# Kernel optimization log

Measured on AMD Instinct MI355X. Metric: run time of the kernel, lower is better.

Reference implementation:

```python
import jax, jax.numpy as jnp
import numpy as np

D_MODEL, N_LEVELS, N_HEADS, N_POINTS = 256, 4, 8, 4
SHAPES = [(100, 100), (50, 50), (25, 25), (13, 13)]  # (H, W) per level


def setup_inputs() -> dict:
    key = jax.random.key(0)
    ks = jax.random.split(key, 8)
    N = 2
    C = D_MODEL
    Len_in = sum(h * w for h, w in SHAPES)
    Lq = Len_in  # encoder self-attention
    query = jax.random.normal(ks[0], (N, Lq, C), jnp.float32)
    reference_points = jax.random.uniform(ks[1], (N, Lq, N_LEVELS, 2), dtype=jnp.float32)
    input_flatten = jax.random.normal(ks[2], (N, Len_in, C), jnp.float32)
    input_spatial_shapes = np.array(SHAPES, dtype=np.int64)
    areas = input_spatial_shapes[:, 0] * input_spatial_shapes[:, 1]
    input_level_start_index = np.concatenate([[0], np.cumsum(areas)[:-1]]).astype(np.int64)
    s = 1.0 / np.sqrt(C)
    Wv = jax.random.uniform(ks[3], (C, C), jnp.float32, -s, s)
    bv = jnp.zeros((C,), jnp.float32)
    # sampling_offsets: small random weight + the module's grid bias init
    Woff = jax.random.normal(ks[4], (N_HEADS * N_LEVELS * N_POINTS * 2, C), jnp.float32) * 0.01
    thetas = jnp.arange(N_HEADS, dtype=jnp.float32) * (2.0 * np.pi / N_HEADS)
    grid = jnp.stack([jnp.cos(thetas), jnp.sin(thetas)], -1)  # (M,2)
    grid = grid / jnp.max(jnp.abs(grid), axis=-1, keepdims=True)
    grid = jnp.tile(grid[:, None, None, :], (1, N_LEVELS, N_POINTS, 1))
    grid = grid * (jnp.arange(N_POINTS, dtype=jnp.float32) + 1.0)[None, None, :, None]
    boff = grid.reshape(-1)
    Wa = jax.random.normal(ks[5], (N_HEADS * N_LEVELS * N_POINTS, C), jnp.float32) * 0.02
    ba = jnp.zeros((N_HEADS * N_LEVELS * N_POINTS,), jnp.float32)
    Wo = jax.random.uniform(ks[6], (C, C), jnp.float32, -s, s)
    bo = jnp.zeros((C,), jnp.float32)
    return {
        'query': query, 'reference_points': reference_points, 'input_flatten': input_flatten,
        'input_spatial_shapes': input_spatial_shapes, 'input_level_start_index': input_level_start_index,
        'Wv': Wv, 'bv': bv, 'Woff': Woff, 'boff': boff, 'Wa': Wa, 'ba': ba, 'Wo': Wo, 'bo': bo,
    }


def _msda_forward(query, reference_points, input_flatten, shapes, starts,
                  Wv, bv, Woff, boff, Wa, ba, Wo, bo):
    N, Lq, C = query.shape
    M, L, P = N_HEADS, N_LEVELS, N_POINTS
    D = C // M
    value = (input_flatten @ Wv.T + bv).reshape(N, -1, M, D)  # (N, Len_in, M, D)
    off = (query @ Woff.T + boff).reshape(N, Lq, M, L, P, 2)
    attn = jax.nn.softmax((query @ Wa.T + ba).reshape(N, Lq, M, L * P), axis=-1)
    attn = attn.reshape(N, Lq, M, L, P)
    # offset_normalizer = (W_l, H_l)
    norm = jnp.asarray(shapes[:, ::-1].copy(), jnp.float32)  # (L, 2)
    loc = reference_points[:, :, None, :, None, :] + off / norm[None, None, None, :, None, :]
    grids = 2.0 * loc - 1.0  # (N, Lq, M, L, P, 2), grid_sample convention
    out = jnp.zeros((N, Lq, M, D), query.dtype)
    for l in range(L):
        H, W = int(shapes[l, 0]), int(shapes[l, 1])
        s0 = int(starts[l])
        v = value[:, s0:s0 + H * W]  # (N, H*W, M, D)
        # align_corners=False unnormalization
        gx = ((grids[:, :, :, l, :, 0] + 1.0) * W - 1.0) / 2.0  # (N, Lq, M, P)
        gy = ((grids[:, :, :, l, :, 1] + 1.0) * H - 1.0) / 2.0
        x0 = jnp.floor(gx); y0 = jnp.floor(gy)
        fx = gx - x0;       fy = gy - y0
        x0i = x0.astype(jnp.int32); y0i = y0.astype(jnp.int32)

        def gather(iy, ix):
            valid = (iy >= 0) & (iy < H) & (ix >= 0) & (ix < W)
            lin = jnp.clip(iy, 0, H - 1) * W + jnp.clip(ix, 0, W - 1)  # (N, Lq, M, P)
            lin2 = lin.transpose(0, 1, 3, 2).reshape(N, Lq * P, M)
            g = jnp.take_along_axis(v, lin2[..., None], axis=1)  # (N, Lq*P, M, D)
            g = g.reshape(N, Lq, P, M, D).transpose(0, 1, 3, 2, 4)  # (N, Lq, M, P, D)
            return g * valid[..., None]  # zero padding outside

        s00 = gather(y0i, x0i)
        s01 = gather(y0i, x0i + 1)
        s10 = gather(y0i + 1, x0i)
        s11 = gather(y0i + 1, x0i + 1)
        sampled = (s00 * ((1 - fy) * (1 - fx))[..., None] + s01 * ((1 - fy) * fx)[..., None]
                   + s10 * (fy * (1 - fx))[..., None] + s11 * (fy * fx)[..., None])
        out = out + jnp.einsum('nqmp,nqmpd->nqmd', attn[:, :, :, l], sampled)
    out = out.reshape(N, Lq, C)
    return out @ Wo.T + bo


def reference(query, reference_points, input_flatten, input_spatial_shapes, input_level_start_index,
              Wv, bv, Woff, boff, Wa, ba, Wo, bo):
    shapes = np.asarray(input_spatial_shapes)
    starts = np.asarray(input_level_start_index)
    return _msda_forward(query, reference_points, input_flatten, shapes, starts,
                         Wv, bv, Woff, boff, Wa, ba, Wo, bo)
```

## Files before the change

### kernel.cpp

```cpp
#include <hip/hip_runtime.h>
#include <math.h>

#define NB   2
#define LQ   13294
#define NROWS (NB*LQ)
#define CDIM 256
#define HSLICES (NROWS + 1)
#define HS32 ((size_t)HSLICES * 32)

typedef unsigned short u16;
typedef unsigned int   u32;
typedef short bf16x8 __attribute__((ext_vector_type(8)));
typedef float f32x4  __attribute__((ext_vector_type(4)));
typedef float f32x2  __attribute__((ext_vector_type(2)));

struct alignas(8) U16x4 { u16 x, y, z, w; };

__device__ __forceinline__ u16 f2bf(float f) {
    u32 u = __builtin_bit_cast(u32, f);
    u += 0x7FFFu + ((u >> 16) & 1u);
    return (u16)(u >> 16);
}

__device__ __forceinline__ u32 cvtpk(float a, float b) {
    u32 d;
    asm("v_cvt_pk_bf16_f32 %0, %1, %2" : "=v"(d) : "v"(a), "v"(b));
    return d;
}

__device__ __forceinline__ void gload_lds16(const void* g, void* l) {
    __builtin_amdgcn_global_load_lds(
        (__attribute__((address_space(1))) void*)g,
        (__attribute__((address_space(3))) void*)l, 16, 0, 0);
}

__device__ __forceinline__ f32x2 bfpair(u32 u) {
    union { u32 w[2]; f32x2 v; } x;
    x.w[0] = u << 16;
    x.w[1] = u & 0xFFFF0000u;
    return x.v;
}

__device__ __forceinline__ void core_f32src(
    const float* __restrict__ A, const float* __restrict__ Bf, int M, int row0,
    u16* As, u16* Bs, f32x4 (&acc)[4][4]) {
    const int tid  = threadIdx.x;
    const int lane = tid & 63;
    const int wave = tid >> 6;
    const int ln16 = lane & 15;
    const int kq   = lane >> 4;
    const int wr   = (wave >> 1) * 64;
    const int wc   = (wave & 1) * 64;

    #pragma unroll
    for (int kt = 0; kt < 4; ++kt) {
        const int k0 = kt * 64;
        #pragma unroll
        for (int it = 0; it < 4; ++it) {
            int chunk = it * 256 + tid;
            int row = chunk >> 3;
            int ch  = chunk & 7;
            int dst = row * 64 + ((ch ^ (row & 7)) * 8);
            int gra = min(row0 + row, M - 1);
            const float* pa = A + (size_t)gra * 256 + k0 + ch * 8;
            float4 a0 = *(const float4*)pa;
            float4 a1 = *(const float4*)(pa + 4);
            uint4 ua;
            ua.x = cvtpk(a0.x, a0.y); ua.y = cvtpk(a0.z, a0.w);
            ua.z = cvtpk(a1.x, a1.y); ua.w = cvtpk(a1.z, a1.w);
            *(uint4*)&As[dst] = ua;
            const float* pb = Bf + (size_t)row * 256 + k0 + ch * 8;
            float4 b0 = *(const float4*)pb;
            float4 b1 = *(const float4*)(pb + 4);
            uint4 ub;
            ub.x = cvtpk(b0.x, b0.y); ub.y = cvtpk(b0.z, b0.w);
            ub.z = cvtpk(b1.x, b1.y); ub.w = cvtpk(b1.z, b1.w);
            *(uint4*)&Bs[dst] = ub;
        }
        __syncthreads();
        #pragma unroll
        for (int kf = 0; kf < 2; ++kf) {
            const int ck = kf * 4 + kq;
            bf16x8 a[4], b[4];
            #pragma unroll
            for (int i = 0; i < 4; ++i) {
                int r = wr + i * 16 + ln16;
                a[i] = *(const bf16x8*)&As[r * 64 + ((ck ^ (r & 7)) * 8)];
                int c = wc + i * 16 + ln16;
                b[i] = *(const bf16x8*)&Bs[c * 64 + ((ck ^ (c & 7)) * 8)];
            }
            #pragma unroll
            for (int i = 0; i < 4; ++i)
                #pragma unroll
                for (int j = 0; j < 4; ++j)
                    acc[i][j] = __builtin_amdgcn_mfma_f32_16x16x32_bf16(
                        a[i], b[j], acc[i][j], 0, 0, 0);
        }
        __syncthreads();
    }
}

__device__ __forceinline__ void core_mixed(
    const u16* __restrict__ A, const float* __restrict__ Bf, int M, int row0,
    u16* As, u16* Bs, f32x4 (&acc)[4][4]) {
    const int tid  = threadIdx.x;
    const int lane = tid & 63;
    const int wave = tid >> 6;
    const int ln16 = lane & 15;
    const int kq   = lane >> 4;
    const int wr   = (wave >> 1) * 64;
    const int wc   = (wave & 1) * 64;

    #pragma unroll
    for (int kt = 0; kt < 4; ++kt) {
        const int k0 = kt * 64;
        #pragma unroll
        for (int it = 0; it < 4; ++it) {
            int chunk = it * 256 + tid;
            int row = chunk >> 3;
            int ch  = chunk & 7;
            int chs = (ch ^ (row & 7)) * 8;
            int gra = min(row0 + row, M - 1);
            gload_lds16(A + (size_t)gra * 256 + k0 + chs, As + chunk * 8);
            const float* pb = Bf + (size_t)row * 256 + k0 + ch * 8;
            float4 b0 = *(const float4*)pb;
            float4 b1 = *(const float4*)(pb + 4);
            uint4 ub;
            ub.x = cvtpk(b0.x, b0.y); ub.y = cvtpk(b0.z, b0.w);
            ub.z = cvtpk(b1.x, b1.y); ub.w = cvtpk(b1.z, b1.w);
            *(uint4*)&Bs[row * 64 + chs] = ub;
        }
        __syncthreads();
        #pragma unroll
        for (int kf = 0; kf < 2; ++kf) {
            const int ck = kf * 4 + kq;
            bf16x8 a[4], b[4];
            #pragma unroll
            for (int i = 0; i < 4; ++i) {
                int r = wr + i * 16 + ln16;
                a[i] = *(const bf16x8*)&As[r * 64 + ((ck ^ (r & 7)) * 8)];
                int c = wc + i * 16 + ln16;
                b[i] = *(const bf16x8*)&Bs[c * 64 + ((ck ^ (c & 7)) * 8)];
            }
            #pragma unroll
            for (int i = 0; i < 4; ++i)
                #pragma unroll
                for (int j = 0; j < 4; ++j)
                    acc[i][j] = __builtin_amdgcn_mfma_f32_16x16x32_bf16(
                        a[i], b[j], acc[i][j], 0, 0, 0);
        }
        __syncthreads();
    }
}

__global__ __launch_bounds__(256, 3)
void gemm_front(const float* __restrict__ query, const float* __restrict__ inflat,
                const float* __restrict__ Wv, const float* __restrict__ Woff,
                const float* __restrict__ Wa, const float* __restrict__ bv,
                const float* __restrict__ boff, const float* __restrict__ ba,
                u16* __restrict__ value, float* __restrict__ offb,
                float* __restrict__ logit, int M) {
    __shared__ u16 As[128 * 64];
    __shared__ u16 Bs[128 * 64];
    const int s    = blockIdx.x;
    const int row0 = blockIdx.y * 128;
    const float* A  = (s < 2) ? inflat : query;
    const float* Bf = (s == 0) ? Wv
                    : (s == 1) ? Wv + 32768
                    : (s == 2) ? Woff
                    : (s == 3) ? Woff + 32768
                    : Wa;
    const float* bias = (s < 2) ? bv + s * 128
                      : (s < 4) ? boff + (s - 2) * 128
                      : ba;

    f32x4 acc[4][4] = {};
    core_f32src(A, Bf, M, row0, As, Bs, acc);

    const int lane = threadIdx.x & 63;
    const int wave = threadIdx.x >> 6;
    const int ln16 = lane & 15, kq = lane >> 4;
    const int wr = (wave >> 1) * 64, wc = (wave & 1) * 64;
    #pragma unroll
    for (int j = 0; j < 4; ++j) {
        int lc = wc + j * 16 + ln16;
        float bj = bias[lc];
        #pragma unroll
        for (int i = 0; i < 4; ++i) {
            #pragma unroll
            for (int r = 0; r < 4; ++r) {
                int gr = row0 + wr + i * 16 + kq * 4 + r;
                if (gr < M) {
                    float o = acc[i][j][r] + bj;
                    if (s < 2) {
                        int c = s * 128 + lc;
                        value[(size_t)(c >> 5) * HS32 + (size_t)gr * 32 + (c & 31)] = f2bf(o);
                    } else if (s < 4)
                        offb[(size_t)gr * 256 + (s - 2) * 128 + lc] = o;
                    else
                        logit[(size_t)gr * 128 + lc] = o;
                }
            }
        }
    }
    if (s == 0 && blockIdx.y == 0) {
        int tt = threadIdx.x;
        value[(size_t)(tt >> 5) * HS32 + (size_t)NROWS * 32 + (tt & 31)] = 0;
    }
}

__global__ __launch_bounds__(256, 3)
void gemm_out(const u16* __restrict__ A, const float* __restrict__ Wo,
              const float* __restrict__ bias, float* __restrict__ C, int M) {
    __shared__ u16 As[128 * 64];
    __shared__ u16 Bs[128 * 64];
    const int s    = blockIdx.x;
    const int row0 = blockIdx.y * 128;
    const float* Bf = Wo + (size_t)s * 32768;

    f32x4 acc[4][4] = {};
    core_mixed(A, Bf, M, row0, As, Bs, acc);

    const int lane = threadIdx.x & 63;
    const int wave = threadIdx.x >> 6;
    const int ln16 = lane & 15, kq = lane >> 4;
    const int wr = (wave >> 1) * 64, wc = (wave & 1) * 64;
    #pragma unroll
    for (int j = 0; j < 4; ++j) {
        int gc = s * 128 + wc + j * 16 + ln16;
        float bj = bias[gc];
        #pragma unroll
        for (int i = 0; i < 4; ++i) {
            #pragma unroll
            for (int r = 0; r < 4; ++r) {
                int gr = row0 + wr + i * 16 + kq * 4 + r;
                if (gr < M) C[(size_t)gr * 256 + gc] = acc[i][j][r] + bj;
            }
        }
    }
}

__global__ __launch_bounds__(256)
void msda_sample(const u16* __restrict__ value,
                 const float* __restrict__ refpts,
                 const float* __restrict__ off,
                 const float* __restrict__ logits,
                 u16* __restrict__ tmp) {
    __shared__ float sAw[4][8][16];
    __shared__ int   sLin[4][8][16][2];
    __shared__ float sW[4][8][16][4];

    const int t  = threadIdx.x;
    const int qb = blockIdx.x * 4;

    if (t < 32) {
        const int qi = t >> 3, m = t & 7;
        const float* lg = logits + (size_t)(qb + qi) * 128 + m * 16;
        float e[16];
        float mx = -1e30f;
        #pragma unroll
        for (int i = 0; i < 16; ++i) { e[i] = lg[i]; mx = fmaxf(mx, e[i]); }
        float s = 0.f;
        #pragma unroll
        for (int i = 0; i < 16; ++i) { e[i] = __expf(e[i] - mx); s += e[i]; }
        const float inv = 1.f / s;
        #pragma unroll
        for (int i = 0; i < 16; ++i) sAw[qi][m][i] = e[i] * inv;
    }
    __syncthreads();

    #pragma unroll
    for (int j2 = 0; j2 < 2; ++j2) {
        const int job = t + j2 * 256;
        const int qi = job >> 7;
        const int m  = (job >> 4) & 7;
        const int p  = job & 15;
        const int l  = p >> 2, pp = p & 3;
        const int q  = qb + qi;
        const int n  = (q >= LQ) ? 1 : 0;

        const int W = (l == 0) ? 100 : (l == 1) ? 50 : (l == 2) ? 25 : 13;
        const int H = W;
        const int st = (l == 0) ? 0 : (l == 1) ? 10000 : (l == 2) ? 12500 : 13125;
        const float invW = (l == 0) ? 0.01f : (l == 1) ? 0.02f
                         : (l == 2) ? 0.04f : (1.f / 13.f);

        const float rx = refpts[(size_t)q * 8 + l * 2 + 0];
        const float ry = refpts[(size_t)q * 8 + l * 2 + 1];
        const float ox = off[(size_t)q * 256 + m * 32 + (l * 4 + pp) * 2 + 0];
        const float oy = off[(size_t)q * 256 + m * 32 + (l * 4 + pp) * 2 + 1];

        const float locx = rx + ox * invW;
        const float locy = ry + oy * invW;
        const float grx = 2.f * locx - 1.f;
        const float gry = 2.f * locy - 1.f;
        const float gx = ((grx + 1.f) * (float)W - 1.f) * 0.5f;
        const float gy = ((gry + 1.f) * (float)H - 1.f) * 0.5f;
        const float x0f = floorf(gx), y0f = floorf(gy);
        const float fx = gx - x0f, fy = gy - y0f;
        const int x0 = (int)x0f, y0 = (int)y0f;
        const int x1 = x0 + 1, y1 = y0 + 1;

        const int cx0 = min(max(x0, 0), W - 1);
        const int cx1 = min(max(x1, 0), W - 1);
        const int cy0 = min(max(y0, 0), H - 1);
        const int cy1 = min(max(y1, 0), H - 1);
        const bool vx0 = (x0 >= 0) & (x0 < W);
        const bool vx1 = (x1 >= 0) & (x1 < W);
        const bool vy0 = (y0 >= 0) & (y0 < H);
        const bool vy1 = (y1 >= 0) & (y1 < H);

        const float aw = sAw[qi][m][p];
        const int base = n * LQ + st;
        const float w00 = (vy0 & vx0) ? aw * (1.f - fy) * (1.f - fx) : 0.f;
        const float w01 = (vy0 & vx1) ? aw * (1.f - fy) * fx         : 0.f;
        const float w10 = (vy1 & vx0) ? aw * fy * (1.f - fx)         : 0.f;
        const float w11 = (vy1 & vx1) ? aw * fy * fx                 : 0.f;
        const bool fold = (x0 < 0);
        sLin[qi][m][p][0] = base + cy0 * W + cx0;
        sLin[qi][m][p][1] = base + cy1 * W + cx0;
        sW[qi][m][p][0] = fold ? w01 : w00;
        sW[qi][m][p][1] = fold ? 0.f : w01;
        sW[qi][m][p][2] = fold ? w11 : w10;
        sW[qi][m][p][3] = fold ? 0.f : w11;
    }
    __syncthreads();

    const int qi = t >> 6;
    const int m  = (t >> 3) & 7;
    const int e  = t & 7;
    const int xh = e >> 2;
    const int c4 = e & 3;
    const int q  = qb + qi;
    const char* vb = (const char*)value + (size_t)m * (HS32 * 2);
    const u32 eoff = (u32)e * 16u;

    f32x2 a2[4] = {{0.f, 0.f}, {0.f, 0.f}, {0.f, 0.f}, {0.f, 0.f}};
    #pragma unroll
    for (int p = 0; p < 16; ++p) {
        int2   rb = *(const int2*)  &sLin[qi][m][p][0];
        float4 w4 = *(const float4*)&sW  [qi][m][p][0];
        uint4 r0 = *(const uint4*)(vb + ((u32)rb.x * 64u + eoff));
        uint4 r1 = *(const uint4*)(vb + ((u32)rb.y * 64u + eoff));
        const float wa = xh ? w4.y : w4.x;
        const float wb_ = xh ? w4.w : w4.z;
        f32x2 wa2 = {wa, wa};
        f32x2 wb2 = {wb_, wb_};
        a2[0] += wa2 * bfpair(r0.x); a2[1] += wa2 * bfpair(r0.y);
        a2[2] += wa2 * bfpair(r0.z); a2[3] += wa2 * bfpair(r0.w);
        a2[0] += wb2 * bfpair(r1.x); a2[1] += wb2 * bfpair(r1.y);
        a2[2] += wb2 * bfpair(r1.z); a2[3] += wb2 * bfpair(r1.w);
    }
    #pragma unroll
    for (int k = 0; k < 4; ++k) {
        a2[k].x += __shfl_xor(a2[k].x, 4);
        a2[k].y += __shfl_xor(a2[k].y, 4);
    }
    if (xh == 0) {
        uint4 o;
        o.x = (u32)f2bf(a2[0].x) | ((u32)f2bf(a2[0].y) << 16);
        o.y = (u32)f2bf(a2[1].x) | ((u32)f2bf(a2[1].y) << 16);
        o.z = (u32)f2bf(a2[2].x) | ((u32)f2bf(a2[2].y) << 16);
        o.w = (u32)f2bf(a2[3].x) | ((u32)f2bf(a2[3].y) << 16);
        *(uint4*)((char*)tmp + ((u32)q * 512u + (u32)m * 64u + (u32)c4 * 16u)) = o;
    }
}

extern "C" void kernel_launch(void* const* d_in, const int* in_sizes, int n_in,
                              void* d_out, int out_size, void* d_ws, size_t ws_size,
                              hipStream_t stream) {
    const float* query  = (const float*)d_in[0];
    const float* refpts = (const float*)d_in[1];
    const float* inflat = (const float*)d_in[2];
    const float* Wv   = (const float*)d_in[5];
    const float* bv   = (const float*)d_in[6];
    const float* Woff = (const float*)d_in[7];
    const float* boff = (const float*)d_in[8];
    const float* Wa   = (const float*)d_in[9];
    const float* ba   = (const float*)d_in[10];
    const float* Wo   = (const float*)d_in[11];
    const float* bo   = (const float*)d_in[12];
    float* out = (float*)d_out;

    char* ws = (char*)d_ws;
    constexpr size_t SZ16  = (size_t)NROWS * 256 * 2;
    constexpr size_t SZVAL = ((size_t)HSLICES * 512 + 4095) & ~(size_t)4095;
    constexpr size_t SZ32  = (size_t)NROWS * 256 * 4;
    u16*   tmp   = (u16*)(ws);
    u16*   value = (u16*)(ws + SZ16);
    float* offb  = (float*)(ws + SZ16 + SZVAL);
    float* logit = (float*)(ws + SZ16 + SZVAL + SZ32);

    const int RG = (NROWS + 127) / 128;

    gemm_front<<<dim3(5, RG), dim3(256), 0, stream>>>(
        query, inflat, Wv, Woff, Wa, bv, boff, ba, value, offb, logit, NROWS);

    hipLaunchKernelGGL(msda_sample, dim3(NROWS / 4), dim3(256), 0, stream,
                       value, refpts, offb, logit, tmp);

    gemm_out<<<dim3(2, RG), dim3(256), 0, stream>>>(
        tmp, Wo, bo, out, NROWS);
}
```

Baseline: 223.3 us.

## Pre-convert inputs and weights to bf16, use async LDS loads in GEMMs

```diff
diff --git a/kernel.cpp b/kernel.cpp
--- a/kernel.cpp
+++ b/kernel.cpp
@@ -22,12 +22,6 @@
     return (u16)(u >> 16);
 }
 
-__device__ __forceinline__ u32 cvtpk(float a, float b) {
-    u32 d;
-    asm("v_cvt_pk_bf16_f32 %0, %1, %2" : "=v"(d) : "v"(a), "v"(b));
-    return d;
-}
-
 __device__ __forceinline__ void gload_lds16(const void* g, void* l) {
     __builtin_amdgcn_global_load_lds(
         (__attribute__((address_space(1))) void*)g,
@@ -41,8 +35,37 @@
     return x.v;
 }
 
-__device__ __forceinline__ void core_f32src(
-    const float* __restrict__ A, const float* __restrict__ Bf, int M, int row0,
+__global__ __launch_bounds__(256)
+void prep_all(const float4* __restrict__ query, const float4* __restrict__ inflat,
+              const float* __restrict__ Wv, const float* __restrict__ Woff,
+              const float* __restrict__ Wa, const float* __restrict__ Wo,
+              u16* __restrict__ qb, u16* __restrict__ ib,
+              u16* __restrict__ wb) {
+    const int b = blockIdx.x;
+    const int t = threadIdx.x;
+    if (b < 6647) {
+        int i = b * 256 + t;
+        float4 v = query[i];
+        U16x4 o{f2bf(v.x), f2bf(v.y), f2bf(v.z), f2bf(v.w)};
+        *(U16x4*)&qb[(size_t)i * 4] = o;
+    } else if (b < 13294) {
+        int i = (b - 6647) * 256 + t;
+        float4 v = inflat[i];
+        U16x4 o{f2bf(v.x), f2bf(v.y), f2bf(v.z), f2bf(v.w)};
+        *(U16x4*)&ib[(size_t)i * 4] = o;
+    } else {
+        int i = (b - 13294) * 256 + t;
+        float v;
+        if      (i <  65536) v = Wv[i];
+        else if (i < 131072) v = Woff[i - 65536];
+        else if (i < 163840) v = Wa[i - 131072];
+        else                 v = Wo[i - 163840];
+        wb[i] = f2bf(v);
+    }
+}
+
+__device__ __forceinline__ void gemm_core128(
+    const u16* __restrict__ A, const u16* __restrict__ Bw, int M, int row0,
     u16* As, u16* Bs, f32x4 (&acc)[4][4]) {
     const int tid  = threadIdx.x;
     const int lane = tid & 63;
@@ -60,22 +83,10 @@
             int chunk = it * 256 + tid;
             int row = chunk >> 3;
             int ch  = chunk & 7;
-            int dst = row * 64 + ((ch ^ (row & 7)) * 8);
+            int chs = (ch ^ (row & 7)) * 8;
             int gra = min(row0 + row, M - 1);
-            const float* pa = A + (size_t)gra * 256 + k0 + ch * 8;
-            float4 a0 = *(const float4*)pa;
-            float4 a1 = *(const float4*)(pa + 4);
-            uint4 ua;
-            ua.x = cvtpk(a0.x, a0.y); ua.y = cvtpk(a0.z, a0.w);
-            ua.z = cvtpk(a1.x, a1.y); ua.w = cvtpk(a1.z, a1.w);
-            *(uint4*)&As[dst] = ua;
-            const float* pb = Bf + (size_t)row * 256 + k0 + ch * 8;
-            float4 b0 = *(const float4*)pb;
-            float4 b1 = *(const float4*)(pb + 4);
-            uint4 ub;
-            ub.x = cvtpk(b0.x, b0.y); ub.y = cvtpk(b0.z, b0.w);
-            ub.z = cvtpk(b1.x, b1.y); ub.w = cvtpk(b1.z, b1.w);
-            *(uint4*)&Bs[dst] = ub;
+            gload_lds16(A  + (size_t)gra * 256 + k0 + chs, As + chunk * 8);
+            gload_lds16(Bw + (size_t)row * 256 + k0 + chs, Bs + chunk * 8);
         }
         __syncthreads();
         #pragma unroll
@@ -100,126 +111,99 @@
     }
 }
 
-__device__ __forceinline__ void core_mixed(
-    const u16* __restrict__ A, const float* __restrict__ Bf, int M, int row0,
-    u16* As, u16* Bs, f32x4 (&acc)[4][4]) {
+__global__ __launch_bounds__(256, 4)
+void gemm_front(const u16* __restrict__ qb, const u16* __restrict__ ib,
+                const u16* __restrict__ wb, const float* __restrict__ bv,
+                const float* __restrict__ boff, const float* __restrict__ ba,
+                u16* __restrict__ value, float* __restrict__ offb,
+                float* __restrict__ logit, int M) {
+    __shared__ u16 Sh[128 * 128];
+    u16* As = Sh;
+    u16* Bs = Sh + 8192;
+    const int s    = blockIdx.x;
+    const int row0 = blockIdx.y * 128;
+    const u16* A  = (s < 2) ? ib : qb;
+    const u16* Bw = wb + (size_t)s * 32768;
+    const float* bias = (s == 0) ? bv
+                      : (s == 1) ? bv + 128
+                      : (s == 2) ? boff
+                      : (s == 3) ? boff + 128
+                      : ba;
+
+    f32x4 acc[4][4] = {};
+    gemm_core128(A, Bw, M, row0, As, Bs, acc);
+
     const int tid  = threadIdx.x;
     const int lane = tid & 63;
     const int wave = tid >> 6;
-    const int ln16 = lane & 15;
-    const int kq   = lane >> 4;
-    const int wr   = (wave >> 1) * 64;
-    const int wc   = (wave & 1) * 64;
-
-    #pragma unroll
-    for (int kt = 0; kt < 4; ++kt) {
-        const int k0 = kt * 64;
-        #pragma unroll
-        for (int it = 0; it < 4; ++it) {
-            int chunk = it * 256 + tid;
-            int row = chunk >> 3;
-            int ch  = chunk & 7;
-            int chs = (ch ^ (row & 7)) * 8;
-            int gra = min(row0 + row, M - 1);
-            gload_lds16(A + (size_t)gra * 256 + k0 + chs, As + chunk * 8);
-            const float* pb = Bf + (size_t)row * 256 + k0 + ch * 8;
-            float4 b0 = *(const float4*)pb;
-            float4 b1 = *(const float4*)(pb + 4);
-            uint4 ub;
-            ub.x = cvtpk(b0.x, b0.y); ub.y = cvtpk(b0.z, b0.w);
-            ub.z = cvtpk(b1.x, b1.y); ub.w = cvtpk(b1.z, b1.w);
-            *(uint4*)&Bs[row * 64 + chs] = ub;
-        }
-        __syncthreads();
-        #pragma unroll
-        for (int kf = 0; kf < 2; ++kf) {
-            const int ck = kf * 4 + kq;
-            bf16x8 a[4], b[4];
-            #pragma unroll
-            for (int i = 0; i < 4; ++i) {
-                int r = wr + i * 16 + ln16;
-                a[i] = *(const bf16x8*)&As[r * 64 + ((ck ^ (r & 7)) * 8)];
-                int c = wc + i * 16 + ln16;
-                b[i] = *(const bf16x8*)&Bs[c * 64 + ((ck ^ (c & 7)) * 8)];
-            }
+    const int ln16 = lane & 15, kq = lane >> 4;
+    const int wr = (wave >> 1) * 64, wc = (wave & 1) * 64;
+
+    if (s < 2) {
+        #pragma unroll
+        for (int j = 0; j < 4; ++j) {
+            int cl = wc + j * 16 + ln16;
+            float bj = bias[cl];
             #pragma unroll
             for (int i = 0; i < 4; ++i)
                 #pragma unroll
-                for (int j = 0; j < 4; ++j)
-                    acc[i][j] = __builtin_amdgcn_mfma_f32_16x16x32_bf16(
-                        a[i], b[j], acc[i][j], 0, 0, 0);
+                for (int r = 0; r < 4; ++r) {
+                    int rl = wr + i * 16 + kq * 4 + r;
+                    Sh[rl * 128 + cl] = f2bf(acc[i][j][r] + bj);
+                }
         }
         __syncthreads();
-    }
-}
-
-__global__ __launch_bounds__(256, 3)
-void gemm_front(const float* __restrict__ query, const float* __restrict__ inflat,
-                const float* __restrict__ Wv, const float* __restrict__ Woff,
-                const float* __restrict__ Wa, const float* __restrict__ bv,
-                const float* __restrict__ boff, const float* __restrict__ ba,
-                u16* __restrict__ value, float* __restrict__ offb,
-                float* __restrict__ logit, int M) {
-    __shared__ u16 As[128 * 64];
-    __shared__ u16 Bs[128 * 64];
+        #pragma unroll
+        for (int it = 0; it < 8; ++it) {
+            int ci = it * 256 + tid;
+            int tr = ci >> 4;
+            int cc = ci & 15;
+            int gr = row0 + tr;
+            if (gr < M) {
+                int cg = s * 128 + cc * 8;
+                u16* dst = value + (size_t)(cg >> 5) * HS32
+                                 + (size_t)gr * 32 + (cg & 31);
+                *(uint4*)dst = *(const uint4*)&Sh[tr * 128 + cc * 8];
+            }
+        }
+        if (s == 0 && blockIdx.y == 0) {
+            value[(size_t)(tid >> 5) * HS32 + (size_t)NROWS * 32 + (tid & 31)] = 0;
+        }
+    } else {
+        #pragma unroll
+        for (int j = 0; j < 4; ++j) {
+            int lc = wc + j * 16 + ln16;
+            float bj = bias[lc];
+            #pragma unroll
+            for (int i = 0; i < 4; ++i) {
+                #pragma unroll
+                for (int r = 0; r < 4; ++r) {
+                    int gr = row0 + wr + i * 16 + kq * 4 + r;
+                    if (gr < M) {
+                        float o = acc[i][j][r] + bj;
+                        if (s < 4)
+                            offb[(size_t)gr * 256 + (s - 2) * 128 + lc] = o;
+                        else
+                            logit[(size_t)gr * 128 + lc] = o;
+                    }
+                }
+            }
+        }
+    }
+}
+
+__global__ __launch_bounds__(256, 4)
+void gemm_out(const u16* __restrict__ A, const u16* __restrict__ Bw0,
+              const float* __restrict__ bias, float* __restrict__ C, int M) {
+    __shared__ u16 Sh[128 * 128];
+    u16* As = Sh;
+    u16* Bs = Sh + 8192;
     const int s    = blockIdx.x;
     const int row0 = blockIdx.y * 128;
-    const float* A  = (s < 2) ? inflat : query;
-    const float* Bf = (s == 0) ? Wv
-                    : (s == 1) ? Wv + 32768
-                    : (s == 2) ? Woff
-                    : (s == 3) ? Woff + 32768
-                    : Wa;
-    const float* bias = (s < 2) ? bv + s * 128
-                      : (s < 4) ? boff + (s - 2) * 128
-                      : ba;
+    const u16* Bw = Bw0 + (size_t)s * 32768;
 
     f32x4 acc[4][4] = {};
-    core_f32src(A, Bf, M, row0, As, Bs, acc);
-
-    const int lane = threadIdx.x & 63;
-    const int wave = threadIdx.x >> 6;
-    const int ln16 = lane & 15, kq = lane >> 4;
-    const int wr = (wave >> 1) * 64, wc = (wave & 1) * 64;
-    #pragma unroll
-    for (int j = 0; j < 4; ++j) {
-        int lc = wc + j * 16 + ln16;
-        float bj = bias[lc];
-        #pragma unroll
-        for (int i = 0; i < 4; ++i) {
-            #pragma unroll
-            for (int r = 0; r < 4; ++r) {
-                int gr = row0 + wr + i * 16 + kq * 4 + r;
-                if (gr < M) {
-                    float o = acc[i][j][r] + bj;
-                    if (s < 2) {
-                        int c = s * 128 + lc;
-                        value[(size_t)(c >> 5) * HS32 + (size_t)gr * 32 + (c & 31)] = f2bf(o);
-                    } else if (s < 4)
-                        offb[(size_t)gr * 256 + (s - 2) * 128 + lc] = o;
-                    else
-                        logit[(size_t)gr * 128 + lc] = o;
-                }
-            }
-        }
-    }
-    if (s == 0 && blockIdx.y == 0) {
-        int tt = threadIdx.x;
-        value[(size_t)(tt >> 5) * HS32 + (size_t)NROWS * 32 + (tt & 31)] = 0;
-    }
-}
-
-__global__ __launch_bounds__(256, 3)
-void gemm_out(const u16* __restrict__ A, const float* __restrict__ Wo,
-              const float* __restrict__ bias, float* __restrict__ C, int M) {
-    __shared__ u16 As[128 * 64];
-    __shared__ u16 Bs[128 * 64];
-    const int s    = blockIdx.x;
-    const int row0 = blockIdx.y * 128;
-    const float* Bf = Wo + (size_t)s * 32768;
-
-    f32x4 acc[4][4] = {};
-    core_mixed(A, Bf, M, row0, As, Bs, acc);
+    gemm_core128(A, Bw, M, row0, As, Bs, acc);
 
     const int lane = threadIdx.x & 63;
     const int wave = threadIdx.x >> 6;
@@ -302,7 +286,6 @@
         const int x1 = x0 + 1, y1 = y0 + 1;
 
         const int cx0 = min(max(x0, 0), W - 1);
-        const int cx1 = min(max(x1, 0), W - 1);
         const int cy0 = min(max(y0, 0), H - 1);
         const int cy1 = min(max(y1, 0), H - 1);
         const bool vx0 = (x0 >= 0) & (x0 < W);
@@ -386,19 +369,27 @@
     constexpr size_t SZ16  = (size_t)NROWS * 256 * 2;
     constexpr size_t SZVAL = ((size_t)HSLICES * 512 + 4095) & ~(size_t)4095;
     constexpr size_t SZ32  = (size_t)NROWS * 256 * 4;
-    u16*   tmp   = (u16*)(ws);
-    u16*   value = (u16*)(ws + SZ16);
-    float* offb  = (float*)(ws + SZ16 + SZVAL);
-    float* logit = (float*)(ws + SZ16 + SZVAL + SZ32);
+    constexpr size_t SZL   = (size_t)NROWS * 128 * 4;
+    u16*   qb    = (u16*)(ws);
+    u16*   ib    = (u16*)(ws + SZ16);
+    u16*   value = (u16*)(ws + 2 * SZ16);
+    float* offb  = (float*)(ws + 2 * SZ16 + SZVAL);
+    float* logit = (float*)(ws + 2 * SZ16 + SZVAL + SZ32);
+    u16*   wb    = (u16*)(ws + 2 * SZ16 + SZVAL + SZ32 + SZL);
+    u16*   tmp   = qb;
 
     const int RG = (NROWS + 127) / 128;
 
+    hipLaunchKernelGGL(prep_all, dim3(14190), dim3(256), 0, stream,
+                       (const float4*)query, (const float4*)inflat,
+                       Wv, Woff, Wa, Wo, qb, ib, wb);
+
     gemm_front<<<dim3(5, RG), dim3(256), 0, stream>>>(
-        query, inflat, Wv, Woff, Wa, bv, boff, ba, value, offb, logit, NROWS);
+        qb, ib, wb, bv, boff, ba, value, offb, logit, NROWS);
 
     hipLaunchKernelGGL(msda_sample, dim3(NROWS / 4), dim3(256), 0, stream,
                        value, refpts, offb, logit, tmp);
 
     gemm_out<<<dim3(2, RG), dim3(256), 0, stream>>>(
-        tmp, Wo, bo, out, NROWS);
-}
+        tmp, wb + 163840, bo, out, NROWS);
+}
```

Measured after the change: 208.8 us. 1.07x faster.
